# Performance work log

Hardware: AMD Instinct MI355X
Metric: run time of the kernel (lower is better)

Reference implementation:

```python
import jax, jax.numpy as jnp
import numpy as np

V_PATCH = (1, 2, 4, 8, 16, 32)
RESI = 0.5   # abs(quant_resi)
BETA = 0.25
K_PHI = 4    # share_quant_resi


def _phi_idx(si, SN, K=K_PHI):
    # PhiPartiallyShared.__getitem__ with at = si/(SN-1)
    ticks = np.linspace(1/3/K, 1 - 1/3/K, K) if K == 4 else np.linspace(1/2/K, 1 - 1/2/K, K)
    return int(np.argmin(np.abs(ticks - si / (SN - 1))))


def _area_down(x, pn):
    # F.interpolate mode='area' with pn | H  == exact block mean
    B, C, H, W = x.shape
    return x.reshape(B, C, pn, H // pn, pn, W // pn).mean(axis=(3, 5))


def _bilinear(x, size):
    # matches torch bilinear, align_corners=False, antialias=False (half-pixel centers)
    B, C, _, _ = x.shape
    return jax.image.resize(x, (B, C, size, size), method='bilinear', antialias=False)


def _down(x, pn, si):
    if pn == x.shape[2]:
        return x
    return _area_down(x, pn) if si <= 3 else _bilinear(x, pn)


def _phi_ada(h, w, b, fw, fb, sn):
    # Phi_ada: conv weight modulated by fc(SN); fc is zero-init but kept in the graph
    C = h.shape[1]
    cond = (fw[:, 0] * jnp.float32(sn) + fb).reshape(C, C, 1, 1)
    wmod = w * (1.0 + cond)
    y = jax.lax.conv_general_dilated(h, wmod, (1, 1), 'SAME',
                                     dimension_numbers=('NCHW', 'OIHW', 'NCHW'))
    y = y + b[None, :, None, None]
    return h * (1.0 - RESI) + y * RESI


def _forward(f, embed_w, conv_w, conv_b, fc_w, fc_b):
    B, C, H, W = f.shape
    SN = len(V_PATCH)
    f_ng = jax.lax.stop_gradient(f)
    f_rest = f_ng
    f_hat = jnp.zeros_like(f_ng)
    e_ng = jax.lax.stop_gradient(embed_w)            # embedding.weight.data
    e_sq = jnp.sum(e_ng * e_ng, axis=1)              # [V]
    vq_losses = []
    commit = jnp.float32(0.0)
    for si, pn in enumerate(V_PATCH):
        rest = f_rest if si == SN - 1 else _down(f_rest, pn, si)
        rest_NC = rest.transpose(0, 2, 3, 1).reshape(-1, C)          # [N,C]
        # squared L2 distances to codebook, argmin (non-differentiable)
        d = (jnp.sum(rest_NC * rest_NC, axis=1, keepdims=True)
             + e_sq - 2.0 * (rest_NC @ e_ng.T))                       # [N,V]
        idx = jnp.argmin(d, axis=1)                                   # [N]
        h = embed_w[idx].reshape(B, pn, pn, C).transpose(0, 3, 1, 2)  # [B,C,pn,pn]
        if si != SN - 1:
            h = _bilinear(h, H)
        k = _phi_idx(si, SN)
        h = _phi_ada(h, conv_w[k], conv_b[k], fc_w[k], fc_b[k], SN)
        f_hat = f_hat + h
        f_rest = f_rest - jax.lax.stop_gradient(h)    # grad through f_rest is killed by argmin anyway
        vq_losses.append(jnp.mean((f_hat - f_ng) ** 2))
        fh_ng = jax.lax.stop_gradient(f_hat)
        commit = commit + jnp.mean((_down(fh_ng, pn, si) - _down(f, pn, si)) ** 2) * BETA
    commit = commit / SN
    # straight-through estimator
    f_hat_out = jax.lax.stop_gradient(f_hat) - f_ng + f
    return f_hat_out, jnp.stack(vq_losses), commit


def setup_inputs() -> dict:
    key = jax.random.key(0)
    k1, k2, k3 = jax.random.split(key, 3)
    B, C, H, W = 32, 64, 32, 32
    V = 4096
    f_BChw = jax.random.normal(k1, (B, C, H, W), dtype=jnp.float32)
    embed_w = jax.random.normal(k2, (V, C), dtype=jnp.float32) * 0.5  # trunc_normal std=0.5
    conv_w = jax.random.normal(k3, (K_PHI, C, C, 3, 3), dtype=jnp.float32) * 0.02
    conv_b = jnp.zeros((K_PHI, C), dtype=jnp.float32)
    fc_w = jnp.zeros((K_PHI, C * C, 1), dtype=jnp.float32)  # Phi_ada.fc zero-init
    fc_b = jnp.zeros((K_PHI, C * C), dtype=jnp.float32)
    return {'f_BChw': f_BChw, 'embed_w': embed_w, 'conv_w': conv_w,
            'conv_b': conv_b, 'fc_w': fc_w, 'fc_b': fc_b}


def reference(f_BChw, embed_w, conv_w, conv_b, fc_w, fc_b):
    return _forward(f_BChw, embed_w, conv_w, conv_b, fc_w, fc_b)
```

## Files before the change

kernel.cpp:

```cpp
#include <hip/hip_runtime.h>
#include <cfloat>

#define N_ELEM 2097152
#define TAU 2.0e-2f

typedef short s16x8 __attribute__((ext_vector_type(8)));
typedef float f32x4 __attribute__((ext_vector_type(4)));

__device__ __forceinline__ unsigned short f2bf(float v) {
    unsigned u = __float_as_uint(v);
    u += 0x7FFFu + ((u >> 16) & 1u);
    return (unsigned short)(u >> 16);
}
__device__ __forceinline__ float bf2f(unsigned short h) {
    return __uint_as_float(((unsigned)h) << 16);
}

__device__ __forceinline__ float blockReduceSum(float v) {
    __shared__ float red[4];
    #pragma unroll
    for (int off = 32; off; off >>= 1) v += __shfl_down(v, off, 64);
    int wid = threadIdx.x >> 6, lane = threadIdx.x & 63;
    if (lane == 0) red[wid] = v;
    __syncthreads();
    float r = 0.f;
    if (threadIdx.x == 0) {
        int nw = ((int)blockDim.x + 63) >> 6;
        for (int w = 0; w < nw; ++w) r += red[w];
    }
    __syncthreads();
    return r;
}

__global__ void k_embprep(const float* __restrict__ e, float* __restrict__ hesq,
                          unsigned short* __restrict__ ehi, unsigned short* __restrict__ elo) {
    int v = blockIdx.x * 256 + threadIdx.x;
    if (v >= 4096) return;
    const float4* r = (const float4*)(e + (size_t)v * 64);
    float s = 0.f;
    #pragma unroll
    for (int i = 0; i < 16; ++i) {
        float4 a = r[i];
        s += a.x * a.x + a.y * a.y + a.z * a.z + a.w * a.w;
    }
    hesq[v] = 0.5f * s;
    for (int i = 0; i < 64; ++i) {
        float x = e[(size_t)v * 64 + i];
        unsigned short h = f2bf(x);
        ehi[(size_t)v * 64 + i] = h;
        elo[(size_t)v * 64 + i] = f2bf(x - bf2f(h));
    }
}

__global__ void k_wmod(const float* __restrict__ w, const float* __restrict__ fcw,
                       const float* __restrict__ fcb,
                       unsigned short* __restrict__ wh, unsigned short* __restrict__ wl) {
    int i = blockIdx.x * 256 + threadIdx.x;
    if (i >= 4 * 64 * 64 * 9) return;
    int k = i / (64 * 64 * 9);
    int r = i % (64 * 64 * 9);
    int oi = r / 9;
    int t = r % 9;
    int co = oi >> 6, ci = oi & 63;
    float cond = fcw[k * 4096 + oi] * 6.0f + fcb[k * 4096 + oi];
    float v = w[i] * (1.0f + cond);
    size_t o = ((size_t)(k * 9 + t) * 64 + co) * 64 + ci;
    unsigned short h = f2bf(v);
    wh[o] = h;
    wl[o] = f2bf(v - bf2f(h));
}

template<bool DIFF>
__global__ void k_pool_wide(const float* __restrict__ A, const float* __restrict__ Bt,
                            float* __restrict__ out, int pn, int s) {
    int o = blockIdx.x;
    int px = o % pn;
    int t1 = o / pn;
    int py = t1 % pn;
    int t2 = t1 / pn;
    int c = t2 % 64, b = t2 / 64;
    size_t base = (((size_t)(b * 64 + c)) * 32 + (size_t)py * s) * 32 + (size_t)px * s;
    float acc = 0.f;
    int tot = s * s;
    for (int i = threadIdx.x; i < tot; i += blockDim.x) {
        int dy = i / s, dx = i % s;
        float v = A[base + dy * 32 + dx];
        if (DIFF) v -= Bt[base + dy * 32 + dx];
        acc += v;
    }
    acc = blockReduceSum(acc);
    if (threadIdx.x == 0) out[o] = acc / (float)tot;
}

template<bool DIFF>
__global__ void k_pool_small(const float* __restrict__ A, const float* __restrict__ Bt,
                             float* __restrict__ out, int pn, int s) {
    int o = blockIdx.x * 256 + threadIdx.x;
    int total = 2048 * pn * pn;
    if (o >= total) return;
    int px = o % pn;
    int t1 = o / pn;
    int py = t1 % pn;
    int t2 = t1 / pn;
    int c = t2 % 64, b = t2 / 64;
    size_t base = (((size_t)(b * 64 + c)) * 32 + (size_t)py * s) * 32 + (size_t)px * s;
    float acc = 0.f;
    for (int dy = 0; dy < s; ++dy)
        for (int dx = 0; dx < s; ++dx) {
            float v = A[base + dy * 32 + dx];
            if (DIFF) v -= Bt[base + dy * 32 + dx];
            acc += v;
        }
    out[o] = acc / (float)(s * s);
}

__global__ void k_trans_nc(const float* __restrict__ src, float* __restrict__ dst,
                           unsigned short* __restrict__ dhi, unsigned short* __restrict__ dlo,
                           int pn2) {
    __shared__ float t[64][65];
    int b = blockIdx.x;
    int p0 = blockIdx.y * 64;
    int lane = threadIdx.x & 63, r4 = threadIdx.x >> 6;
    #pragma unroll
    for (int i = 0; i < 16; ++i) {
        int c = i * 4 + r4;
        t[c][lane] = src[((size_t)b * 64 + c) * pn2 + p0 + lane];
    }
    __syncthreads();
    #pragma unroll
    for (int i = 0; i < 16; ++i) {
        int p = i * 4 + r4;
        size_t o = ((size_t)(b * pn2 + p0 + p)) * 64 + lane;
        float v = t[lane][p];
        unsigned short h = f2bf(v);
        dst[o] = v;
        dhi[o] = h;
        dlo[o] = f2bf(v - bf2f(h));
    }
}

__global__ void k_trans_small(const float* __restrict__ src, float* __restrict__ dst,
                              unsigned short* __restrict__ dhi, unsigned short* __restrict__ dlo,
                              int pn2) {
    int i = blockIdx.x * 256 + threadIdx.x;
    int total = 2048 * pn2;
    if (i >= total) return;
    int c = i & 63, n = i >> 6;
    int b = n / pn2, p = n % pn2;
    float v = src[((size_t)b * 64 + c) * pn2 + p];
    unsigned short h = f2bf(v);
    dst[i] = v;
    dhi[i] = h;
    dlo[i] = f2bf(v - bf2f(h));
}

__global__ __launch_bounds__(256) void k_vq_mfma(
        const unsigned short* __restrict__ resthi, const unsigned short* __restrict__ restlo,
        const unsigned short* __restrict__ embhi,  const unsigned short* __restrict__ emblo,
        const float* __restrict__ hesq,
        float* __restrict__ m1v_, int* __restrict__ m1i_,
        float* __restrict__ m2v_, int* __restrict__ m2i_,
        int N, int CPS) {
    __shared__ __align__(16) unsigned short lah[64 * 64];
    __shared__ __align__(16) unsigned short lal[64 * 64];
    __shared__ __align__(16) float lq[64];
    int tid = threadIdx.x;
    int lane = tid & 63, wv = tid >> 6;
    int split = blockIdx.y;
    int p0 = blockIdx.x * 64 + wv * 16;
    int pt = p0 + (lane & 15);
    int ptc = min(pt, N - 1);
    int ko8 = (lane >> 4) * 8;

    const unsigned short* rb = resthi + (size_t)ptc * 64;
    const unsigned short* rl = restlo + (size_t)ptc * 64;
    s16x8 bh0 = *(const s16x8*)(rb + ko8);
    s16x8 bh1 = *(const s16x8*)(rb + 32 + ko8);
    s16x8 bl0 = *(const s16x8*)(rl + ko8);
    s16x8 bl1 = *(const s16x8*)(rl + 32 + ko8);

    float m1v = FLT_MAX, m2v = FLT_MAX;
    int m1i = 0, m2i = 0;

    int cbeg = split * CPS;
    for (int oc = 0; oc < CPS; oc += 64) {
        int cb = cbeg + oc;
        __syncthreads();
        for (int t = tid; t < 512; t += 256) {
            int cc = t >> 3, part = t & 7;
            int bo = (cc * 128 + part * 16) ^ ((cc & 7) << 4);
            *(uint4*)((char*)lah + bo) = *(const uint4*)(embhi + (size_t)(cb + cc) * 64 + part * 8);
            *(uint4*)((char*)lal + bo) = *(const uint4*)(emblo + (size_t)(cb + cc) * 64 + part * 8);
        }
        if (tid < 64) lq[tid] = hesq[cb + tid];
        __syncthreads();
        #pragma unroll
        for (int sub = 0; sub < 4; ++sub) {
            int cl = sub * 16 + (lane & 15);
            int sw = (cl & 7) << 4;
            int rowb = cl * 128;
            s16x8 ah0 = *(const s16x8*)((const char*)lah + ((rowb + ko8 * 2) ^ sw));
            s16x8 ah1 = *(const s16x8*)((const char*)lah + ((rowb + 64 + ko8 * 2) ^ sw));
            s16x8 al0 = *(const s16x8*)((const char*)lal + ((rowb + ko8 * 2) ^ sw));
            s16x8 al1 = *(const s16x8*)((const char*)lal + ((rowb + 64 + ko8 * 2) ^ sw));
            f32x4 acc = {0.f, 0.f, 0.f, 0.f};
            acc = __builtin_amdgcn_mfma_f32_16x16x32_bf16(ah0, bh0, acc, 0, 0, 0);
            acc = __builtin_amdgcn_mfma_f32_16x16x32_bf16(ah1, bh1, acc, 0, 0, 0);
            acc = __builtin_amdgcn_mfma_f32_16x16x32_bf16(ah0, bl0, acc, 0, 0, 0);
            acc = __builtin_amdgcn_mfma_f32_16x16x32_bf16(ah1, bl1, acc, 0, 0, 0);
            acc = __builtin_amdgcn_mfma_f32_16x16x32_bf16(al0, bh0, acc, 0, 0, 0);
            acc = __builtin_amdgcn_mfma_f32_16x16x32_bf16(al1, bh1, acc, 0, 0, 0);
            int crow = cb + sub * 16 + (lane >> 4) * 4;
            f32x4 q = *(const f32x4*)(lq + sub * 16 + (lane >> 4) * 4);
            #pragma unroll
            for (int r = 0; r < 4; ++r) {
                float s = q[r] - acc[r];
                int c = crow + r;
                bool lt1 = s < m1v, lt2 = s < m2v;
                float nm2v = lt2 ? s : m2v; int nm2i = lt2 ? c : m2i;
                nm2v = lt1 ? m1v : nm2v;    nm2i = lt1 ? m1i : nm2i;
                m1v = lt1 ? s : m1v;        m1i = lt1 ? c : m1i;
                m2v = nm2v; m2i = nm2i;
            }
        }
    }
    #pragma unroll
    for (int off = 16; off <= 32; off <<= 1) {
        float o1v = __shfl_xor(m1v, off, 64); int o1i = __shfl_xor(m1i, off, 64);
        float o2v = __shfl_xor(m2v, off, 64); int o2i = __shfl_xor(m2i, off, 64);
        if (o1v < m1v) {
            float c2v = (m1v < o2v) ? m1v : o2v; int c2i = (m1v < o2v) ? m1i : o2i;
            m1v = o1v; m1i = o1i; m2v = c2v; m2i = c2i;
        } else if (o1v < m2v) {
            m2v = o1v; m2i = o1i;
        }
    }
    if ((lane >> 4) == 0 && pt < N) {
        size_t o = (size_t)split * N + pt;
        m1v_[o] = m1v; m1i_[o] = m1i; m2v_[o] = m2v; m2i_[o] = m2i;
    }
}

__global__ void k_vq_combine(const float* __restrict__ m1v_, const int* __restrict__ m1i_,
                             const float* __restrict__ m2v_, const int* __restrict__ m2i_,
                             int* __restrict__ idx, int* __restrict__ flag, int* __restrict__ count,
                             int N, int SPLITS) {
    int n = blockIdx.x * 256 + threadIdx.x;
    if (n >= N) return;
    float a1v = m1v_[n], a2v = m2v_[n];
    int a1i = m1i_[n], a2i = m2i_[n];
    for (int s = 1; s < SPLITS; ++s) {
        size_t o = (size_t)s * N + n;
        float b1v = m1v_[o], b2v = m2v_[o];
        int b1i = m1i_[o], b2i = m2i_[o];
        if (b1v < a1v) {
            float c2v = (a1v < b2v) ? a1v : b2v; int c2i = (a1v < b2v) ? a1i : b2i;
            a1v = b1v; a1i = b1i; a2v = c2v; a2i = c2i;
        } else if (b1v < a2v) {
            a2v = b1v; a2i = b1i;
        }
    }
    idx[n] = a1i;
    if (a2v - a1v < TAU) {
        int p = atomicAdd(count, 1);
        flag[p] = n;
    }
}

__global__ __launch_bounds__(256) void k_vq_exact(
        const float* __restrict__ restnc, const float* __restrict__ embed,
        const float* __restrict__ hesq, const int* __restrict__ flag,
        const int* __restrict__ count, unsigned long long* __restrict__ pmin) {
    __shared__ float rs[32 * 64];
    __shared__ unsigned long long red[4];
    int tid = threadIdx.x;
    int lane = tid & 63, wv = tid >> 6;
    int cnt = *count;
    int nb = (cnt + 31) >> 5;
    int ntask = nb * 16;
    for (int task = blockIdx.x; task < ntask; task += gridDim.x) {
        int batch = task >> 4, spl = task & 15;
        int lbase = batch << 5;
        int npts = min(32, cnt - lbase);
        __syncthreads();
        for (int i = tid; i < npts * 64; i += 256) {
            int li = i >> 6;
            rs[i] = restnc[(size_t)flag[lbase + li] * 64 + (i & 63)];
        }
        __syncthreads();
        int code = spl * 256 + tid;
        const float4* e4 = (const float4*)(embed + (size_t)code * 64);
        float4 e[16];
        #pragma unroll
        for (int i = 0; i < 16; ++i) e[i] = e4[i];
        float hq = hesq[code];
        for (int p = 0; p < npts; ++p) {
            const float4* r4 = (const float4*)(rs + p * 64);
            float d0 = 0.f, d1 = 0.f, d2 = 0.f, d3 = 0.f;
            #pragma unroll
            for (int i = 0; i < 16; i += 4) {
                float4 e0 = e[i], e1 = e[i + 1], e2 = e[i + 2], e3 = e[i + 3];
                d0 += e0.x * r4[i].x     + e0.y * r4[i].y     + e0.z * r4[i].z     + e0.w * r4[i].w;
                d1 += e1.x * r4[i + 1].x + e1.y * r4[i + 1].y + e1.z * r4[i + 1].z + e1.w * r4[i + 1].w;
                d2 += e2.x * r4[i + 2].x + e2.y * r4[i + 2].y + e2.z * r4[i + 2].z + e2.w * r4[i + 2].w;
                d3 += e3.x * r4[i + 3].x + e3.y * r4[i + 3].y + e3.z * r4[i + 3].z + e3.w * r4[i + 3].w;
            }
            float s = hq - ((d0 + d1) + (d2 + d3));
            unsigned u = __float_as_uint(s);
            u = (u & 0x80000000u) ? ~u : (u | 0x80000000u);
            unsigned long long pk = (((unsigned long long)u) << 32) | (unsigned)code;
            #pragma unroll
            for (int off = 32; off; off >>= 1) {
                unsigned long long o = __shfl_down(pk, off, 64);
                if (o < pk) pk = o;
            }
            if (lane == 0) red[wv] = pk;
            __syncthreads();
            if (tid == 0) {
                unsigned long long m = red[0];
                for (int w = 1; w < 4; ++w) if (red[w] < m) m = red[w];
                atomicMin(pmin + flag[lbase + p], m);
            }
            __syncthreads();
        }
    }
}

__global__ void k_gather(const int* __restrict__ idx, const unsigned long long* __restrict__ pmin,
                         const float* __restrict__ embed, float* __restrict__ hs, int N) {
    int i = blockIdx.x * 256 + threadIdx.x;
    if (i >= N * 64) return;
    int n = i >> 6, c = i & 63;
    unsigned long long pv = pmin[n];
    int id = (pv != 0xFFFFFFFFFFFFFFFFull) ? (int)(pv & 0xFFFFFFFFull) : idx[n];
    hs[i] = embed[(size_t)id * 64 + c];
}

__global__ void k_upsample(const float* __restrict__ hs, float* __restrict__ hupf,
                           unsigned short* __restrict__ huph, unsigned short* __restrict__ hupl,
                           int pn) {
    int i = blockIdx.x * 256 + threadIdx.x;
    if (i >= N_ELEM) return;
    int c = i & 63, x = (i >> 6) & 31, y = (i >> 11) & 31, b = i >> 16;
    float scale = (float)pn * (1.0f / 32.0f);
    float sy = (y + 0.5f) * scale - 0.5f;
    float sx = (x + 0.5f) * scale - 0.5f;
    float fy0 = floorf(sy), fx0 = floorf(sx);
    float wy = sy - fy0, wx = sx - fx0;
    int y0 = max(0, min(pn - 1, (int)fy0));
    int y1 = max(0, min(pn - 1, (int)fy0 + 1));
    int x0 = max(0, min(pn - 1, (int)fx0));
    int x1 = max(0, min(pn - 1, (int)fx0 + 1));
    const float* hb = hs + (size_t)b * pn * pn * 64 + c;
    float v00 = hb[(size_t)(y0 * pn + x0) * 64];
    float v01 = hb[(size_t)(y0 * pn + x1) * 64];
    float v10 = hb[(size_t)(y1 * pn + x0) * 64];
    float v11 = hb[(size_t)(y1 * pn + x1) * 64];
    float v = (1.f - wy) * ((1.f - wx) * v00 + wx * v01) + wy * ((1.f - wx) * v10 + wx * v11);
    hupf[i] = v;
    unsigned short h = f2bf(v);
    huph[i] = h;
    hupl[i] = f2bf(v - bf2f(h));
}

__global__ void k_hilo(const float* __restrict__ hs,
                       unsigned short* __restrict__ huph, unsigned short* __restrict__ hupl) {
    int i = blockIdx.x * 256 + threadIdx.x;
    if (i >= N_ELEM) return;
    float v = hs[i];
    unsigned short h = f2bf(v);
    huph[i] = h;
    hupl[i] = f2bf(v - bf2f(h));
}

__global__ __launch_bounds__(256) void k_conv_mfma(
        const unsigned short* __restrict__ huph, const unsigned short* __restrict__ hupl,
        const float* __restrict__ hupf,
        const unsigned short* __restrict__ wh, const unsigned short* __restrict__ wl,
        const float* __restrict__ bias, const float* __restrict__ f_in,
        float* __restrict__ f_hat, float* __restrict__ f_rest,
        float* __restrict__ vq_part) {
    __shared__ __align__(16) unsigned short Xh[6 * 34 * 64];
    __shared__ __align__(16) unsigned short Xl[6 * 34 * 64];
    int b = blockIdx.x, rg = blockIdx.y;
    int y0 = rg * 4;
    int tid = threadIdx.x;
    int lane = tid & 63, wv = tid >> 6;
    int co0 = wv * 16;
    int cr = lane & 15, oct = lane >> 4;

    for (int q = tid; q < 6 * 34 * 8; q += 256) {
        int pl = q >> 3, o8 = q & 7;
        int lr = pl / 34, lc = pl % 34;
        int gy = y0 + lr - 1, gx = lc - 1;
        int bo = (pl * 128 + o8 * 16) ^ ((lc & 7) << 4);
        uint4 vh = {0, 0, 0, 0}, vl = {0, 0, 0, 0};
        if (gy >= 0 && gy < 32 && gx >= 0 && gx < 32) {
            size_t g = (((size_t)(b * 32 + gy)) * 32 + gx) * 64 + o8 * 8;
            vh = *(const uint4*)(huph + g);
            vl = *(const uint4*)(hupl + g);
        }
        *(uint4*)((char*)Xh + bo) = vh;
        *(uint4*)((char*)Xl + bo) = vl;
    }
    __syncthreads();

    f32x4 acc[8];
    #pragma unroll
    for (int ps = 0; ps < 8; ++ps) acc[ps] = (f32x4){0.f, 0.f, 0.f, 0.f};

    for (int t = 0; t < 9; ++t) {
        int dy = t / 3, dx = t % 3;
        #pragma unroll
        for (int cc = 0; cc < 2; ++cc) {
            size_t wo = ((size_t)t * 64 + co0 + cr) * 64 + cc * 32 + oct * 8;
            s16x8 Ah = *(const s16x8*)(wh + wo);
            s16x8 Al = *(const s16x8*)(wl + wo);
            #pragma unroll
            for (int ps = 0; ps < 8; ++ps) {
                int px = ps * 16 + cr;
                int lr = (px >> 5) + dy;
                int lc = (px & 31) + dx;
                int bo = ((lr * 34 + lc) * 128 + cc * 64 + oct * 16) ^ ((lc & 7) << 4);
                s16x8 Bh = *(const s16x8*)((const char*)Xh + bo);
                s16x8 Bl = *(const s16x8*)((const char*)Xl + bo);
                acc[ps] = __builtin_amdgcn_mfma_f32_16x16x32_bf16(Ah, Bh, acc[ps], 0, 0, 0);
                acc[ps] = __builtin_amdgcn_mfma_f32_16x16x32_bf16(Ah, Bl, acc[ps], 0, 0, 0);
                acc[ps] = __builtin_amdgcn_mfma_f32_16x16x32_bf16(Al, Bh, acc[ps], 0, 0, 0);
                acc[ps] = __builtin_amdgcn_mfma_f32_16x16x32_bf16(Al, Bl, acc[ps], 0, 0, 0);
            }
        }
    }

    const float* hupb = hupf + (size_t)b * 65536;
    float local = 0.f;
    #pragma unroll
    for (int ps = 0; ps < 8; ++ps) {
        int px = ps * 16 + cr;
        int y = y0 + (px >> 5), x = px & 31;
        #pragma unroll
        for (int r = 0; r < 4; ++r) {
            int co = co0 + oct * 4 + r;
            float hv = hupb[(size_t)(y * 32 + x) * 64 + co];
            float hconv = acc[ps][r] + bias[co];
            float hout = 0.5f * hv + 0.5f * hconv;
            size_t o = (((size_t)(b * 64 + co)) * 32 + y) * 32 + x;
            float fh = f_hat[o] + hout;
            f_hat[o] = fh;
            f_rest[o] -= hout;
            float d = fh - f_in[o];
            local += d * d;
        }
    }
    local = blockReduceSum(local);
    if (tid == 0) vq_part[b * 8 + rg] = local;
}

__global__ void k_sqsum(const float* __restrict__ v, float* __restrict__ part, int M) {
    float local = 0.f;
    for (int i = blockIdx.x * 256 + threadIdx.x; i < M; i += gridDim.x * 256) {
        float a = v[i];
        local += a * a;
    }
    local = blockReduceSum(local);
    if (threadIdx.x == 0) part[blockIdx.x] = local;
}

__global__ void k_final(const float* __restrict__ vqp, const float* __restrict__ cmp,
                        float* __restrict__ out) {
    const int pn2s[6] = {1, 4, 16, 64, 256, 1024};
    float commit = 0.f;
    for (int si = 0; si < 6; ++si) {
        float l = (threadIdx.x < 256) ? vqp[si * 256 + threadIdx.x] : 0.f;
        l = blockReduceSum(l);
        if (threadIdx.x == 0) out[N_ELEM + si] = l / (float)N_ELEM;

        float csum = 0.f;
        for (int i = threadIdx.x; i < 512; i += 256) csum += cmp[si * 512 + i];
        csum = blockReduceSum(csum);
        if (threadIdx.x == 0) commit += csum / (float)(2048 * pn2s[si]) * 0.25f;
    }
    if (threadIdx.x == 0) out[N_ELEM + 6] = commit / 6.0f;
}

extern "C" void kernel_launch(void* const* d_in, const int* in_sizes, int n_in,
                              void* d_out, int out_size, void* d_ws, size_t ws_size,
                              hipStream_t stream) {
    const float* f     = (const float*)d_in[0];
    const float* embed = (const float*)d_in[1];
    const float* convw = (const float*)d_in[2];
    const float* convb = (const float*)d_in[3];
    const float* fcw   = (const float*)d_in[4];
    const float* fcb   = (const float*)d_in[5];
    float* out = (float*)d_out;
    float* ws  = (float*)d_ws;

    float* f_rest  = ws;
    float* poolhup = ws + 2097152;
    float* restnc  = ws + 4194304;
    float* hs      = restnc;
    unsigned short* resthi = (unsigned short*)(ws + 6291456);
    unsigned short* restlo = (unsigned short*)(ws + 7340032);
    unsigned short* huph   = resthi;
    unsigned short* hupl   = restlo;
    unsigned short* embhi  = (unsigned short*)(ws + 8388608);
    unsigned short* emblo  = (unsigned short*)(ws + 8519680);
    unsigned short* wmodh  = (unsigned short*)(ws + 8650752);
    unsigned short* wmodl  = (unsigned short*)(ws + 8724480);
    float* hesq   = ws + 8798208;
    float* m1v    = ws + 8802304;
    float* m2v    = ws + 8867840;
    int*   m1i    = (int*)(ws + 8933376);
    int*   m2i    = (int*)(ws + 8998912);
    int*   idx    = (int*)(ws + 9064448);
    int*   flag   = (int*)(ws + 9097216);
    int*   count  = (int*)(ws + 9129984);
    unsigned long long* pmin = (unsigned long long*)(ws + 9130048);
    float* vqp    = ws + 9195584;
    float* cmp    = ws + 9197120;

    hipMemsetAsync(d_out, 0, (size_t)out_size * sizeof(float), stream);
    hipMemcpyAsync(f_rest, f, (size_t)N_ELEM * sizeof(float), hipMemcpyDeviceToDevice, stream);
    k_wmod<<<(147456 + 255) / 256, 256, 0, stream>>>(convw, fcw, fcb, wmodh, wmodl);
    k_embprep<<<16, 256, 0, stream>>>(embed, hesq, embhi, emblo);

    const int pns[6]    = {1, 2, 4, 8, 16, 32};
    const int splits[6] = {64, 32, 16, 8, 4, 2};
    const int kidx[6]   = {0, 0, 1, 2, 3, 3};

    for (int si = 0; si < 6; ++si) {
        int pn = pns[si], s = 32 / pn, pn2 = pn * pn;
        int N = 32 * pn2, SPL = splits[si], CPS = 4096 / SPL;
        float* pooled = poolhup;
        float* hupf = poolhup;

        if (si <= 2) {
            k_pool_wide<false><<<2048 * pn2, (s >= 16 ? 256 : 64), 0, stream>>>(f_rest, nullptr, pooled, pn, s);
            k_trans_small<<<(N * 64 + 255) / 256, 256, 0, stream>>>(pooled, restnc, resthi, restlo, pn2);
        } else if (si <= 4) {
            k_pool_small<false><<<(2048 * pn2 + 255) / 256, 256, 0, stream>>>(f_rest, nullptr, pooled, pn, s);
            k_trans_nc<<<dim3(32, pn2 / 64), 256, 0, stream>>>(pooled, restnc, resthi, restlo, pn2);
        } else {
            k_trans_nc<<<dim3(32, 16), 256, 0, stream>>>(f_rest, restnc, resthi, restlo, 1024);
        }

        hipMemsetAsync(count, 0, sizeof(int), stream);
        hipMemsetAsync(pmin, 0xFF, (size_t)N * 8, stream);
        k_vq_mfma<<<dim3((N + 63) / 64, SPL), 256, 0, stream>>>(resthi, restlo, embhi, emblo, hesq,
                                                                m1v, m1i, m2v, m2i, N, CPS);
        k_vq_combine<<<(N + 255) / 256, 256, 0, stream>>>(m1v, m1i, m2v, m2i, idx, flag, count, N, SPL);
        k_vq_exact<<<1024, 256, 0, stream>>>(restnc, embed, hesq, flag, count, pmin);

        k_gather<<<(N * 64 + 255) / 256, 256, 0, stream>>>(idx, pmin, embed, hs, N);
        if (si < 5) {
            k_upsample<<<(N_ELEM + 255) / 256, 256, 0, stream>>>(hs, hupf, huph, hupl, pn);
        } else {
            k_hilo<<<(N_ELEM + 255) / 256, 256, 0, stream>>>(hs, huph, hupl);
            hupf = hs;
        }

        k_conv_mfma<<<dim3(32, 8), 256, 0, stream>>>(huph, hupl, hupf,
                                                     wmodh + kidx[si] * 36864, wmodl + kidx[si] * 36864,
                                                     convb + kidx[si] * 64, f, out, f_rest,
                                                     vqp + si * 256);

        if (si <= 2) k_pool_wide<true><<<2048 * pn2, (s >= 16 ? 256 : 64), 0, stream>>>(out, f, pooled, pn, s);
        else         k_pool_small<true><<<(2048 * pn2 + 255) / 256, 256, 0, stream>>>(out, f, pooled, pn, s);
        k_sqsum<<<512, 256, 0, stream>>>(pooled, cmp + si * 512, 2048 * pn2);
    }

    k_final<<<1, 256, 0, stream>>>(vqp, cmp, out);
}
```

Before: 715.9 us.

## Fuse residual computation, gather/upsample, commit reductions; widen VQ tile to two point groups

```diff
diff --git a/kernel.cpp b/kernel.cpp
--- a/kernel.cpp
+++ b/kernel.cpp
@@ -33,7 +33,7 @@
 }
 
 __global__ void k_embprep(const float* __restrict__ e, float* __restrict__ hesq,
-                          unsigned short* __restrict__ ehi, unsigned short* __restrict__ elo) {
+                          unsigned short* __restrict__ ehiN, unsigned short* __restrict__ eloN) {
     int v = blockIdx.x * 256 + threadIdx.x;
     if (v >= 4096) return;
     const float4* r = (const float4*)(e + (size_t)v * 64);
@@ -47,16 +47,22 @@
     for (int i = 0; i < 64; ++i) {
         float x = e[(size_t)v * 64 + i];
         unsigned short h = f2bf(x);
-        ehi[(size_t)v * 64 + i] = h;
-        elo[(size_t)v * 64 + i] = f2bf(x - bf2f(h));
+        ehiN[(size_t)v * 64 + i] = h ^ 0x8000u;
+        eloN[(size_t)v * 64 + i] = f2bf(x - bf2f(h)) ^ 0x8000u;
     }
 }
 
 __global__ void k_wmod(const float* __restrict__ w, const float* __restrict__ fcw,
                        const float* __restrict__ fcb,
-                       unsigned short* __restrict__ wh, unsigned short* __restrict__ wl) {
+                       unsigned short* __restrict__ wh, unsigned short* __restrict__ wl,
+                       int* __restrict__ count, float* __restrict__ cmpA) {
+    if (blockIdx.x == 576) {
+        int t = threadIdx.x;
+        for (int j = t; j < 384; j += 256) cmpA[j] = 0.f;
+        if (t < 6) count[t] = 0;
+        return;
+    }
     int i = blockIdx.x * 256 + threadIdx.x;
-    if (i >= 4 * 64 * 64 * 9) return;
     int k = i / (64 * 64 * 9);
     int r = i % (64 * 64 * 9);
     int oi = r / 9;
@@ -70,9 +76,9 @@
     wl[o] = f2bf(v - bf2f(h));
 }
 
-template<bool DIFF>
-__global__ void k_pool_wide(const float* __restrict__ A, const float* __restrict__ Bt,
-                            float* __restrict__ out, int pn, int s) {
+__global__ void k_down_wide(const float* __restrict__ f, const float* __restrict__ fhat,
+                            float* __restrict__ restnc, unsigned short* __restrict__ dhi,
+                            unsigned short* __restrict__ dlo, int pn, int s) {
     int o = blockIdx.x;
     int px = o % pn;
     int t1 = o / pn;
@@ -84,16 +90,21 @@
     int tot = s * s;
     for (int i = threadIdx.x; i < tot; i += blockDim.x) {
         int dy = i / s, dx = i % s;
-        float v = A[base + dy * 32 + dx];
-        if (DIFF) v -= Bt[base + dy * 32 + dx];
-        acc += v;
+        acc += f[base + dy * 32 + dx] - fhat[base + dy * 32 + dx];
     }
     acc = blockReduceSum(acc);
-    if (threadIdx.x == 0) out[o] = acc / (float)tot;
-}
-
-template<bool DIFF>
-__global__ void k_pool_small(const float* __restrict__ A, const float* __restrict__ Bt,
+    if (threadIdx.x == 0) {
+        float v = acc / (float)tot;
+        int n = (b * pn + py) * pn + px;
+        size_t oo = (size_t)n * 64 + c;
+        unsigned short h = f2bf(v);
+        restnc[oo] = v;
+        dhi[oo] = h;
+        dlo[oo] = f2bf(v - bf2f(h));
+    }
+}
+
+__global__ void k_pool_small(const float* __restrict__ f, const float* __restrict__ fhat,
                              float* __restrict__ out, int pn, int s) {
     int o = blockIdx.x * 256 + threadIdx.x;
     int total = 2048 * pn * pn;
@@ -106,15 +117,14 @@
     size_t base = (((size_t)(b * 64 + c)) * 32 + (size_t)py * s) * 32 + (size_t)px * s;
     float acc = 0.f;
     for (int dy = 0; dy < s; ++dy)
-        for (int dx = 0; dx < s; ++dx) {
-            float v = A[base + dy * 32 + dx];
-            if (DIFF) v -= Bt[base + dy * 32 + dx];
-            acc += v;
-        }
+        for (int dx = 0; dx < s; ++dx)
+            acc += f[base + dy * 32 + dx] - fhat[base + dy * 32 + dx];
     out[o] = acc / (float)(s * s);
 }
 
-__global__ void k_trans_nc(const float* __restrict__ src, float* __restrict__ dst,
+template<bool DIFF>
+__global__ void k_trans_nc(const float* __restrict__ A, const float* __restrict__ Bt,
+                           float* __restrict__ dst,
                            unsigned short* __restrict__ dhi, unsigned short* __restrict__ dlo,
                            int pn2) {
     __shared__ float t[64][65];
@@ -124,7 +134,10 @@
     #pragma unroll
     for (int i = 0; i < 16; ++i) {
         int c = i * 4 + r4;
-        t[c][lane] = src[((size_t)b * 64 + c) * pn2 + p0 + lane];
+        size_t g = ((size_t)b * 64 + c) * pn2 + p0 + lane;
+        float v = A[g];
+        if (DIFF) v -= Bt[g];
+        t[c][lane] = v;
     }
     __syncthreads();
     #pragma unroll
@@ -139,27 +152,11 @@
     }
 }
 
-__global__ void k_trans_small(const float* __restrict__ src, float* __restrict__ dst,
-                              unsigned short* __restrict__ dhi, unsigned short* __restrict__ dlo,
-                              int pn2) {
-    int i = blockIdx.x * 256 + threadIdx.x;
-    int total = 2048 * pn2;
-    if (i >= total) return;
-    int c = i & 63, n = i >> 6;
-    int b = n / pn2, p = n % pn2;
-    float v = src[((size_t)b * 64 + c) * pn2 + p];
-    unsigned short h = f2bf(v);
-    dst[i] = v;
-    dhi[i] = h;
-    dlo[i] = f2bf(v - bf2f(h));
-}
-
 __global__ __launch_bounds__(256) void k_vq_mfma(
         const unsigned short* __restrict__ resthi, const unsigned short* __restrict__ restlo,
-        const unsigned short* __restrict__ embhi,  const unsigned short* __restrict__ emblo,
+        const unsigned short* __restrict__ embhiN, const unsigned short* __restrict__ embloN,
         const float* __restrict__ hesq,
-        float* __restrict__ m1v_, int* __restrict__ m1i_,
-        float* __restrict__ m2v_, int* __restrict__ m2i_,
+        float* __restrict__ m1v_, int* __restrict__ m1i_, float* __restrict__ m2v_,
         int N, int CPS) {
     __shared__ __align__(16) unsigned short lah[64 * 64];
     __shared__ __align__(16) unsigned short lal[64 * 64];
@@ -167,20 +164,27 @@
     int tid = threadIdx.x;
     int lane = tid & 63, wv = tid >> 6;
     int split = blockIdx.y;
-    int p0 = blockIdx.x * 64 + wv * 16;
-    int pt = p0 + (lane & 15);
-    int ptc = min(pt, N - 1);
-    int ko8 = (lane >> 4) * 8;
-
-    const unsigned short* rb = resthi + (size_t)ptc * 64;
-    const unsigned short* rl = restlo + (size_t)ptc * 64;
-    s16x8 bh0 = *(const s16x8*)(rb + ko8);
-    s16x8 bh1 = *(const s16x8*)(rb + 32 + ko8);
-    s16x8 bl0 = *(const s16x8*)(rl + ko8);
-    s16x8 bl1 = *(const s16x8*)(rl + 32 + ko8);
-
-    float m1v = FLT_MAX, m2v = FLT_MAX;
-    int m1i = 0, m2i = 0;
+    int p0 = blockIdx.x * 128 + wv * 32;
+    int cr = lane & 15, oct = lane >> 4;
+    int ko8 = oct * 8;
+    int ptA = p0 + cr, ptB = p0 + 16 + cr;
+    int pA = min(ptA, N - 1), pB = min(ptB, N - 1);
+
+    const unsigned short* ra = resthi + (size_t)pA * 64;
+    const unsigned short* la = restlo + (size_t)pA * 64;
+    const unsigned short* rb = resthi + (size_t)pB * 64;
+    const unsigned short* lb = restlo + (size_t)pB * 64;
+    s16x8 bhA0 = *(const s16x8*)(ra + ko8);
+    s16x8 bhA1 = *(const s16x8*)(ra + 32 + ko8);
+    s16x8 blA0 = *(const s16x8*)(la + ko8);
+    s16x8 blA1 = *(const s16x8*)(la + 32 + ko8);
+    s16x8 bhB0 = *(const s16x8*)(rb + ko8);
+    s16x8 bhB1 = *(const s16x8*)(rb + 32 + ko8);
+    s16x8 blB0 = *(const s16x8*)(lb + ko8);
+    s16x8 blB1 = *(const s16x8*)(lb + 32 + ko8);
+
+    float m1vA = FLT_MAX, m2vA = FLT_MAX; int m1iA = 0;
+    float m1vB = FLT_MAX, m2vB = FLT_MAX; int m1iB = 0;
 
     int cbeg = split * CPS;
     for (int oc = 0; oc < CPS; oc += 64) {
@@ -189,78 +193,94 @@
         for (int t = tid; t < 512; t += 256) {
             int cc = t >> 3, part = t & 7;
             int bo = (cc * 128 + part * 16) ^ ((cc & 7) << 4);
-            *(uint4*)((char*)lah + bo) = *(const uint4*)(embhi + (size_t)(cb + cc) * 64 + part * 8);
-            *(uint4*)((char*)lal + bo) = *(const uint4*)(emblo + (size_t)(cb + cc) * 64 + part * 8);
+            *(uint4*)((char*)lah + bo) = *(const uint4*)(embhiN + (size_t)(cb + cc) * 64 + part * 8);
+            *(uint4*)((char*)lal + bo) = *(const uint4*)(embloN + (size_t)(cb + cc) * 64 + part * 8);
         }
         if (tid < 64) lq[tid] = hesq[cb + tid];
         __syncthreads();
         #pragma unroll
         for (int sub = 0; sub < 4; ++sub) {
-            int cl = sub * 16 + (lane & 15);
+            int cl = sub * 16 + cr;
             int sw = (cl & 7) << 4;
             int rowb = cl * 128;
             s16x8 ah0 = *(const s16x8*)((const char*)lah + ((rowb + ko8 * 2) ^ sw));
             s16x8 ah1 = *(const s16x8*)((const char*)lah + ((rowb + 64 + ko8 * 2) ^ sw));
             s16x8 al0 = *(const s16x8*)((const char*)lal + ((rowb + ko8 * 2) ^ sw));
             s16x8 al1 = *(const s16x8*)((const char*)lal + ((rowb + 64 + ko8 * 2) ^ sw));
-            f32x4 acc = {0.f, 0.f, 0.f, 0.f};
-            acc = __builtin_amdgcn_mfma_f32_16x16x32_bf16(ah0, bh0, acc, 0, 0, 0);
-            acc = __builtin_amdgcn_mfma_f32_16x16x32_bf16(ah1, bh1, acc, 0, 0, 0);
-            acc = __builtin_amdgcn_mfma_f32_16x16x32_bf16(ah0, bl0, acc, 0, 0, 0);
-            acc = __builtin_amdgcn_mfma_f32_16x16x32_bf16(ah1, bl1, acc, 0, 0, 0);
-            acc = __builtin_amdgcn_mfma_f32_16x16x32_bf16(al0, bh0, acc, 0, 0, 0);
-            acc = __builtin_amdgcn_mfma_f32_16x16x32_bf16(al1, bh1, acc, 0, 0, 0);
-            int crow = cb + sub * 16 + (lane >> 4) * 4;
-            f32x4 q = *(const f32x4*)(lq + sub * 16 + (lane >> 4) * 4);
+            f32x4 q = *(const f32x4*)(lq + sub * 16 + oct * 4);
+            int crow = cb + sub * 16 + oct * 4;
+            f32x4 acc = q;
+            acc = __builtin_amdgcn_mfma_f32_16x16x32_bf16(ah0, bhA0, acc, 0, 0, 0);
+            acc = __builtin_amdgcn_mfma_f32_16x16x32_bf16(ah1, bhA1, acc, 0, 0, 0);
+            acc = __builtin_amdgcn_mfma_f32_16x16x32_bf16(ah0, blA0, acc, 0, 0, 0);
+            acc = __builtin_amdgcn_mfma_f32_16x16x32_bf16(ah1, blA1, acc, 0, 0, 0);
+            acc = __builtin_amdgcn_mfma_f32_16x16x32_bf16(al0, bhA0, acc, 0, 0, 0);
+            acc = __builtin_amdgcn_mfma_f32_16x16x32_bf16(al1, bhA1, acc, 0, 0, 0);
             #pragma unroll
             for (int r = 0; r < 4; ++r) {
-                float s = q[r] - acc[r];
-                int c = crow + r;
-                bool lt1 = s < m1v, lt2 = s < m2v;
-                float nm2v = lt2 ? s : m2v; int nm2i = lt2 ? c : m2i;
-                nm2v = lt1 ? m1v : nm2v;    nm2i = lt1 ? m1i : nm2i;
-                m1v = lt1 ? s : m1v;        m1i = lt1 ? c : m1i;
-                m2v = nm2v; m2i = nm2i;
+                float s = acc[r]; int c = crow + r;
+                bool lt1 = s < m1vA, lt2 = s < m2vA;
+                float nm2 = lt2 ? s : m2vA;
+                m2vA = lt1 ? m1vA : nm2;
+                m1iA = lt1 ? c : m1iA;
+                m1vA = lt1 ? s : m1vA;
+            }
+            f32x4 accB = q;
+            accB = __builtin_amdgcn_mfma_f32_16x16x32_bf16(ah0, bhB0, accB, 0, 0, 0);
+            accB = __builtin_amdgcn_mfma_f32_16x16x32_bf16(ah1, bhB1, accB, 0, 0, 0);
+            accB = __builtin_amdgcn_mfma_f32_16x16x32_bf16(ah0, blB0, accB, 0, 0, 0);
+            accB = __builtin_amdgcn_mfma_f32_16x16x32_bf16(ah1, blB1, accB, 0, 0, 0);
+            accB = __builtin_amdgcn_mfma_f32_16x16x32_bf16(al0, bhB0, accB, 0, 0, 0);
+            accB = __builtin_amdgcn_mfma_f32_16x16x32_bf16(al1, bhB1, accB, 0, 0, 0);
+            #pragma unroll
+            for (int r = 0; r < 4; ++r) {
+                float s = accB[r]; int c = crow + r;
+                bool lt1 = s < m1vB, lt2 = s < m2vB;
+                float nm2 = lt2 ? s : m2vB;
+                m2vB = lt1 ? m1vB : nm2;
+                m1iB = lt1 ? c : m1iB;
+                m1vB = lt1 ? s : m1vB;
             }
         }
     }
     #pragma unroll
     for (int off = 16; off <= 32; off <<= 1) {
-        float o1v = __shfl_xor(m1v, off, 64); int o1i = __shfl_xor(m1i, off, 64);
-        float o2v = __shfl_xor(m2v, off, 64); int o2i = __shfl_xor(m2i, off, 64);
-        if (o1v < m1v) {
-            float c2v = (m1v < o2v) ? m1v : o2v; int c2i = (m1v < o2v) ? m1i : o2i;
-            m1v = o1v; m1i = o1i; m2v = c2v; m2i = c2i;
-        } else if (o1v < m2v) {
-            m2v = o1v; m2i = o1i;
-        }
-    }
-    if ((lane >> 4) == 0 && pt < N) {
-        size_t o = (size_t)split * N + pt;
-        m1v_[o] = m1v; m1i_[o] = m1i; m2v_[o] = m2v; m2i_[o] = m2i;
+        float o1 = __shfl_xor(m1vA, off, 64); int oi = __shfl_xor(m1iA, off, 64);
+        float o2 = __shfl_xor(m2vA, off, 64);
+        if (o1 < m1vA) { m2vA = fminf(m1vA, o2); m1vA = o1; m1iA = oi; }
+        else if (o1 < m2vA) m2vA = o1;
+        o1 = __shfl_xor(m1vB, off, 64); oi = __shfl_xor(m1iB, off, 64);
+        o2 = __shfl_xor(m2vB, off, 64);
+        if (o1 < m1vB) { m2vB = fminf(m1vB, o2); m1vB = o1; m1iB = oi; }
+        else if (o1 < m2vB) m2vB = o1;
+    }
+    if (oct == 0) {
+        if (ptA < N) { size_t o = (size_t)split * N + ptA; m1v_[o] = m1vA; m1i_[o] = m1iA; m2v_[o] = m2vA; }
+        if (ptB < N) { size_t o = (size_t)split * N + ptB; m1v_[o] = m1vB; m1i_[o] = m1iB; m2v_[o] = m2vB; }
     }
 }
 
 __global__ void k_vq_combine(const float* __restrict__ m1v_, const int* __restrict__ m1i_,
-                             const float* __restrict__ m2v_, const int* __restrict__ m2i_,
+                             const float* __restrict__ m2v_,
                              int* __restrict__ idx, int* __restrict__ flag, int* __restrict__ count,
-                             int N, int SPLITS) {
+                             unsigned long long* __restrict__ pmin, int N, int SPLITS) {
     int n = blockIdx.x * 256 + threadIdx.x;
     if (n >= N) return;
     float a1v = m1v_[n], a2v = m2v_[n];
-    int a1i = m1i_[n], a2i = m2i_[n];
+    int a1i = m1i_[n];
     for (int s = 1; s < SPLITS; ++s) {
         size_t o = (size_t)s * N + n;
         float b1v = m1v_[o], b2v = m2v_[o];
-        int b1i = m1i_[o], b2i = m2i_[o];
+        int b1i = m1i_[o];
         if (b1v < a1v) {
-            float c2v = (a1v < b2v) ? a1v : b2v; int c2i = (a1v < b2v) ? a1i : b2i;
-            a1v = b1v; a1i = b1i; a2v = c2v; a2i = c2i;
+            a2v = fminf(a1v, b2v);
+            a1v = b1v; a1i = b1i;
         } else if (b1v < a2v) {
-            a2v = b1v; a2i = b1i;
+            a2v = b1v;
         }
     }
     idx[n] = a1i;
+    pmin[n] = 0xFFFFFFFFFFFFFFFFull;
     if (a2v - a1v < TAU) {
         int p = atomicAdd(count, 1);
         flag[p] = n;
@@ -272,9 +292,8 @@
         const float* __restrict__ hesq, const int* __restrict__ flag,
         const int* __restrict__ count, unsigned long long* __restrict__ pmin) {
     __shared__ float rs[32 * 64];
-    __shared__ unsigned long long red[4];
     int tid = threadIdx.x;
-    int lane = tid & 63, wv = tid >> 6;
+    int lane = tid & 63;
     int cnt = *count;
     int nb = (cnt + 31) >> 5;
     int ntask = nb * 16;
@@ -314,60 +333,49 @@
                 unsigned long long o = __shfl_down(pk, off, 64);
                 if (o < pk) pk = o;
             }
-            if (lane == 0) red[wv] = pk;
-            __syncthreads();
-            if (tid == 0) {
-                unsigned long long m = red[0];
-                for (int w = 1; w < 4; ++w) if (red[w] < m) m = red[w];
-                atomicMin(pmin + flag[lbase + p], m);
-            }
-            __syncthreads();
-        }
-    }
-}
-
-__global__ void k_gather(const int* __restrict__ idx, const unsigned long long* __restrict__ pmin,
-                         const float* __restrict__ embed, float* __restrict__ hs, int N) {
-    int i = blockIdx.x * 256 + threadIdx.x;
-    if (i >= N * 64) return;
-    int n = i >> 6, c = i & 63;
-    unsigned long long pv = pmin[n];
-    int id = (pv != 0xFFFFFFFFFFFFFFFFull) ? (int)(pv & 0xFFFFFFFFull) : idx[n];
-    hs[i] = embed[(size_t)id * 64 + c];
-}
-
-__global__ void k_upsample(const float* __restrict__ hs, float* __restrict__ hupf,
-                           unsigned short* __restrict__ huph, unsigned short* __restrict__ hupl,
-                           int pn) {
+            if (lane == 0) atomicMin(pmin + flag[lbase + p], pk);
+        }
+    }
+}
+
+__global__ void k_up(const int* __restrict__ idx, const unsigned long long* __restrict__ pmin,
+                     const float* __restrict__ embed, float* __restrict__ hupf,
+                     unsigned short* __restrict__ huph, unsigned short* __restrict__ hupl,
+                     int pn) {
     int i = blockIdx.x * 256 + threadIdx.x;
     if (i >= N_ELEM) return;
     int c = i & 63, x = (i >> 6) & 31, y = (i >> 11) & 31, b = i >> 16;
-    float scale = (float)pn * (1.0f / 32.0f);
-    float sy = (y + 0.5f) * scale - 0.5f;
-    float sx = (x + 0.5f) * scale - 0.5f;
-    float fy0 = floorf(sy), fx0 = floorf(sx);
-    float wy = sy - fy0, wx = sx - fx0;
-    int y0 = max(0, min(pn - 1, (int)fy0));
-    int y1 = max(0, min(pn - 1, (int)fy0 + 1));
-    int x0 = max(0, min(pn - 1, (int)fx0));
-    int x1 = max(0, min(pn - 1, (int)fx0 + 1));
-    const float* hb = hs + (size_t)b * pn * pn * 64 + c;
-    float v00 = hb[(size_t)(y0 * pn + x0) * 64];
-    float v01 = hb[(size_t)(y0 * pn + x1) * 64];
-    float v10 = hb[(size_t)(y1 * pn + x0) * 64];
-    float v11 = hb[(size_t)(y1 * pn + x1) * 64];
-    float v = (1.f - wy) * ((1.f - wx) * v00 + wx * v01) + wy * ((1.f - wx) * v10 + wx * v11);
+    float v;
+    if (pn == 32) {
+        int n = (b * 32 + y) * 32 + x;
+        unsigned long long pv = pmin[n];
+        int id = (pv != 0xFFFFFFFFFFFFFFFFull) ? (int)(pv & 0xFFFFFFFFull) : idx[n];
+        v = embed[(size_t)id * 64 + c];
+    } else {
+        float scale = (float)pn * (1.0f / 32.0f);
+        float sy = (y + 0.5f) * scale - 0.5f;
+        float sx = (x + 0.5f) * scale - 0.5f;
+        float fy0 = floorf(sy), fx0 = floorf(sx);
+        float wy = sy - fy0, wx = sx - fx0;
+        int y0 = max(0, min(pn - 1, (int)fy0));
+        int y1 = max(0, min(pn - 1, (int)fy0 + 1));
+        int x0 = max(0, min(pn - 1, (int)fx0));
+        int x1 = max(0, min(pn - 1, (int)fx0 + 1));
+        int nb_ = b * pn * pn;
+        int n00 = nb_ + y0 * pn + x0, n01 = nb_ + y0 * pn + x1;
+        int n10 = nb_ + y1 * pn + x0, n11 = nb_ + y1 * pn + x1;
+        unsigned long long p00 = pmin[n00], p01 = pmin[n01], p10 = pmin[n10], p11 = pmin[n11];
+        int i00 = (p00 != 0xFFFFFFFFFFFFFFFFull) ? (int)(p00 & 0xFFFFFFFFull) : idx[n00];
+        int i01 = (p01 != 0xFFFFFFFFFFFFFFFFull) ? (int)(p01 & 0xFFFFFFFFull) : idx[n01];
+        int i10 = (p10 != 0xFFFFFFFFFFFFFFFFull) ? (int)(p10 & 0xFFFFFFFFull) : idx[n10];
+        int i11 = (p11 != 0xFFFFFFFFFFFFFFFFull) ? (int)(p11 & 0xFFFFFFFFull) : idx[n11];
+        float v00 = embed[(size_t)i00 * 64 + c];
+        float v01 = embed[(size_t)i01 * 64 + c];
+        float v10 = embed[(size_t)i10 * 64 + c];
+        float v11 = embed[(size_t)i11 * 64 + c];
+        v = (1.f - wy) * ((1.f - wx) * v00 + wx * v01) + wy * ((1.f - wx) * v10 + wx * v11);
+    }
     hupf[i] = v;
-    unsigned short h = f2bf(v);
-    huph[i] = h;
-    hupl[i] = f2bf(v - bf2f(h));
-}
-
-__global__ void k_hilo(const float* __restrict__ hs,
-                       unsigned short* __restrict__ huph, unsigned short* __restrict__ hupl) {
-    int i = blockIdx.x * 256 + threadIdx.x;
-    if (i >= N_ELEM) return;
-    float v = hs[i];
     unsigned short h = f2bf(v);
     huph[i] = h;
     hupl[i] = f2bf(v - bf2f(h));
@@ -378,8 +386,7 @@
         const float* __restrict__ hupf,
         const unsigned short* __restrict__ wh, const unsigned short* __restrict__ wl,
         const float* __restrict__ bias, const float* __restrict__ f_in,
-        float* __restrict__ f_hat, float* __restrict__ f_rest,
-        float* __restrict__ vq_part) {
+        float* __restrict__ f_hat, float* __restrict__ vq_part) {
     __shared__ __align__(16) unsigned short Xh[6 * 34 * 64];
     __shared__ __align__(16) unsigned short Xl[6 * 34 * 64];
     int b = blockIdx.x, rg = blockIdx.y;
@@ -447,7 +454,6 @@
             size_t o = (((size_t)(b * 64 + co)) * 32 + y) * 32 + x;
             float fh = f_hat[o] + hout;
             f_hat[o] = fh;
-            f_rest[o] -= hout;
             float d = fh - f_in[o];
             local += d * d;
         }
@@ -456,31 +462,73 @@
     if (tid == 0) vq_part[b * 8 + rg] = local;
 }
 
-__global__ void k_sqsum(const float* __restrict__ v, float* __restrict__ part, int M) {
-    float local = 0.f;
-    for (int i = blockIdx.x * 256 + threadIdx.x; i < M; i += gridDim.x * 256) {
-        float a = v[i];
-        local += a * a;
-    }
-    local = blockReduceSum(local);
-    if (threadIdx.x == 0) part[blockIdx.x] = local;
-}
-
-__global__ void k_final(const float* __restrict__ vqp, const float* __restrict__ cmp,
+__global__ void k_commit_wide(const float* __restrict__ fhat, const float* __restrict__ f,
+                              float* __restrict__ cmp, int pn, int s) {
+    int o = blockIdx.x;
+    int px = o % pn;
+    int t1 = o / pn;
+    int py = t1 % pn;
+    int t2 = t1 / pn;
+    int c = t2 % 64, b = t2 / 64;
+    size_t base = (((size_t)(b * 64 + c)) * 32 + (size_t)py * s) * 32 + (size_t)px * s;
+    float acc = 0.f;
+    int tot = s * s;
+    for (int i = threadIdx.x; i < tot; i += blockDim.x) {
+        int dy = i / s, dx = i % s;
+        acc += fhat[base + dy * 32 + dx] - f[base + dy * 32 + dx];
+    }
+    acc = blockReduceSum(acc);
+    if (threadIdx.x == 0) {
+        float m = acc / (float)tot;
+        atomicAdd(cmp + (blockIdx.x & 63), m * m);
+    }
+}
+
+__global__ void k_commit_small(const float* __restrict__ fhat, const float* __restrict__ f,
+                               float* __restrict__ cmp, int pn, int s) {
+    int o = blockIdx.x * 256 + threadIdx.x;
+    int total = 2048 * pn * pn;
+    float m2 = 0.f;
+    if (o < total) {
+        int px = o % pn;
+        int t1 = o / pn;
+        int py = t1 % pn;
+        int t2 = t1 / pn;
+        int c = t2 % 64, b = t2 / 64;
+        size_t base = (((size_t)(b * 64 + c)) * 32 + (size_t)py * s) * 32 + (size_t)px * s;
+        float acc = 0.f;
+        for (int dy = 0; dy < s; ++dy)
+            for (int dx = 0; dx < s; ++dx)
+                acc += fhat[base + dy * 32 + dx] - f[base + dy * 32 + dx];
+        float m = acc / (float)(s * s);
+        m2 = m * m;
+    }
+    m2 = blockReduceSum(m2);
+    if (threadIdx.x == 0) atomicAdd(cmp + (blockIdx.x & 63), m2);
+}
+
+__global__ void k_final(const float* __restrict__ vqp, const float* __restrict__ cmpA,
                         float* __restrict__ out) {
-    const int pn2s[6] = {1, 4, 16, 64, 256, 1024};
-    float commit = 0.f;
+    const int pn2s[5] = {1, 4, 16, 64, 256};
+    __shared__ float commit_s;
+    if (threadIdx.x == 0) commit_s = 0.f;
+    __syncthreads();
     for (int si = 0; si < 6; ++si) {
-        float l = (threadIdx.x < 256) ? vqp[si * 256 + threadIdx.x] : 0.f;
+        float l = vqp[si * 256 + threadIdx.x];
         l = blockReduceSum(l);
-        if (threadIdx.x == 0) out[N_ELEM + si] = l / (float)N_ELEM;
-
-        float csum = 0.f;
-        for (int i = threadIdx.x; i < 512; i += 256) csum += cmp[si * 512 + i];
-        csum = blockReduceSum(csum);
-        if (threadIdx.x == 0) commit += csum / (float)(2048 * pn2s[si]) * 0.25f;
-    }
-    if (threadIdx.x == 0) out[N_ELEM + 6] = commit / 6.0f;
+        if (threadIdx.x == 0) {
+            float vl = l / (float)N_ELEM;
+            out[N_ELEM + si] = vl;
+            if (si == 5) commit_s += vl * 0.25f;
+        }
+        if (si < 5) {
+            float csum = (threadIdx.x < 64) ? cmpA[si * 64 + threadIdx.x] : 0.f;
+            csum = blockReduceSum(csum);
+            if (threadIdx.x == 0) commit_s += csum / (float)(2048 * pn2s[si]) * 0.25f;
+        }
+    }
+    __syncthreads();
+    if (threadIdx.x == 0) out[N_ELEM + 6] = commit_s / 6.0f;
 }
 
 extern "C" void kernel_launch(void* const* d_in, const int* in_sizes, int n_in,
@@ -495,79 +543,63 @@
     float* out = (float*)d_out;
     float* ws  = (float*)d_ws;
 
-    float* f_rest  = ws;
-    float* poolhup = ws + 2097152;
-    float* restnc  = ws + 4194304;
-    float* hs      = restnc;
-    unsigned short* resthi = (unsigned short*)(ws + 6291456);
-    unsigned short* restlo = (unsigned short*)(ws + 7340032);
+    float* hupf   = ws;
+    float* restnc = ws + 2097152;
+    unsigned short* resthi = (unsigned short*)(ws + 4194304);
+    unsigned short* restlo = (unsigned short*)(ws + 5242880);
     unsigned short* huph   = resthi;
     unsigned short* hupl   = restlo;
-    unsigned short* embhi  = (unsigned short*)(ws + 8388608);
-    unsigned short* emblo  = (unsigned short*)(ws + 8519680);
-    unsigned short* wmodh  = (unsigned short*)(ws + 8650752);
-    unsigned short* wmodl  = (unsigned short*)(ws + 8724480);
-    float* hesq   = ws + 8798208;
-    float* m1v    = ws + 8802304;
-    float* m2v    = ws + 8867840;
-    int*   m1i    = (int*)(ws + 8933376);
-    int*   m2i    = (int*)(ws + 8998912);
-    int*   idx    = (int*)(ws + 9064448);
-    int*   flag   = (int*)(ws + 9097216);
-    int*   count  = (int*)(ws + 9129984);
-    unsigned long long* pmin = (unsigned long long*)(ws + 9130048);
-    float* vqp    = ws + 9195584;
-    float* cmp    = ws + 9197120;
+    unsigned short* embhiN = (unsigned short*)(ws + 6291456);
+    unsigned short* embloN = (unsigned short*)(ws + 6422528);
+    unsigned short* wmodh  = (unsigned short*)(ws + 6553600);
+    unsigned short* wmodl  = (unsigned short*)(ws + 6627328);
+    float* hesq   = ws + 6701056;
+    float* m1v    = ws + 6705152;
+    float* m2v    = ws + 6836224;
+    int*   m1i    = (int*)(ws + 6967296);
+    int*   idx    = (int*)(ws + 7098368);
+    int*   flag   = (int*)(ws + 7131136);
+    int*   count  = (int*)(ws + 7163904);
+    unsigned long long* pmin = (unsigned long long*)(ws + 7163968);
+    float* vqp    = ws + 7229504;
+    float* cmpA   = ws + 7231040;
 
     hipMemsetAsync(d_out, 0, (size_t)out_size * sizeof(float), stream);
-    hipMemcpyAsync(f_rest, f, (size_t)N_ELEM * sizeof(float), hipMemcpyDeviceToDevice, stream);
-    k_wmod<<<(147456 + 255) / 256, 256, 0, stream>>>(convw, fcw, fcb, wmodh, wmodl);
-    k_embprep<<<16, 256, 0, stream>>>(embed, hesq, embhi, emblo);
+    k_wmod<<<577, 256, 0, stream>>>(convw, fcw, fcb, wmodh, wmodl, count, cmpA);
+    k_embprep<<<16, 256, 0, stream>>>(embed, hesq, embhiN, embloN);
 
     const int pns[6]    = {1, 2, 4, 8, 16, 32};
-    const int splits[6] = {64, 32, 16, 8, 4, 2};
+    const int splits[6] = {64, 64, 32, 16, 8, 4};
     const int kidx[6]   = {0, 0, 1, 2, 3, 3};
 
     for (int si = 0; si < 6; ++si) {
         int pn = pns[si], s = 32 / pn, pn2 = pn * pn;
         int N = 32 * pn2, SPL = splits[si], CPS = 4096 / SPL;
-        float* pooled = poolhup;
-        float* hupf = poolhup;
+        float* pooled = hupf;
 
         if (si <= 2) {
-            k_pool_wide<false><<<2048 * pn2, (s >= 16 ? 256 : 64), 0, stream>>>(f_rest, nullptr, pooled, pn, s);
-            k_trans_small<<<(N * 64 + 255) / 256, 256, 0, stream>>>(pooled, restnc, resthi, restlo, pn2);
+            k_down_wide<<<2048 * pn2, (s == 32 ? 256 : 64), 0, stream>>>(f, out, restnc, resthi, restlo, pn, s);
         } else if (si <= 4) {
-            k_pool_small<false><<<(2048 * pn2 + 255) / 256, 256, 0, stream>>>(f_rest, nullptr, pooled, pn, s);
-            k_trans_nc<<<dim3(32, pn2 / 64), 256, 0, stream>>>(pooled, restnc, resthi, restlo, pn2);
+            k_pool_small<<<(2048 * pn2 + 255) / 256, 256, 0, stream>>>(f, out, pooled, pn, s);
+            k_trans_nc<false><<<dim3(32, pn2 / 64), 256, 0, stream>>>(pooled, nullptr, restnc, resthi, restlo, pn2);
         } else {
-            k_trans_nc<<<dim3(32, 16), 256, 0, stream>>>(f_rest, restnc, resthi, restlo, 1024);
-        }
-
-        hipMemsetAsync(count, 0, sizeof(int), stream);
-        hipMemsetAsync(pmin, 0xFF, (size_t)N * 8, stream);
-        k_vq_mfma<<<dim3((N + 63) / 64, SPL), 256, 0, stream>>>(resthi, restlo, embhi, emblo, hesq,
-                                                                m1v, m1i, m2v, m2i, N, CPS);
-        k_vq_combine<<<(N + 255) / 256, 256, 0, stream>>>(m1v, m1i, m2v, m2i, idx, flag, count, N, SPL);
-        k_vq_exact<<<1024, 256, 0, stream>>>(restnc, embed, hesq, flag, count, pmin);
-
-        k_gather<<<(N * 64 + 255) / 256, 256, 0, stream>>>(idx, pmin, embed, hs, N);
-        if (si < 5) {
-            k_upsample<<<(N_ELEM + 255) / 256, 256, 0, stream>>>(hs, hupf, huph, hupl, pn);
-        } else {
-            k_hilo<<<(N_ELEM + 255) / 256, 256, 0, stream>>>(hs, huph, hupl);
-            hupf = hs;
-        }
+            k_trans_nc<true><<<dim3(32, 16), 256, 0, stream>>>(f, out, restnc, resthi, restlo, 1024);
+        }
+
+        k_vq_mfma<<<dim3((N + 127) / 128, SPL), 256, 0, stream>>>(resthi, restlo, embhiN, embloN, hesq,
+                                                                  m1v, m1i, m2v, N, CPS);
+        k_vq_combine<<<(N + 255) / 256, 256, 0, stream>>>(m1v, m1i, m2v, idx, flag, count + si, pmin, N, SPL);
+        k_vq_exact<<<512, 256, 0, stream>>>(restnc, embed, hesq, flag, count + si, pmin);
+
+        k_up<<<(N_ELEM + 255) / 256, 256, 0, stream>>>(idx, pmin, embed, hupf, huph, hupl, pn);
 
         k_conv_mfma<<<dim3(32, 8), 256, 0, stream>>>(huph, hupl, hupf,
                                                      wmodh + kidx[si] * 36864, wmodl + kidx[si] * 36864,
-                                                     convb + kidx[si] * 64, f, out, f_rest,
-                                                     vqp + si * 256);
-
-        if (si <= 2) k_pool_wide<true><<<2048 * pn2, (s >= 16 ? 256 : 64), 0, stream>>>(out, f, pooled, pn, s);
-        else         k_pool_small<true><<<(2048 * pn2 + 255) / 256, 256, 0, stream>>>(out, f, pooled, pn, s);
-        k_sqsum<<<512, 256, 0, stream>>>(pooled, cmp + si * 512, 2048 * pn2);
-    }
-
-    k_final<<<1, 256, 0, stream>>>(vqp, cmp, out);
-}
+                                                     convb + kidx[si] * 64, f, out, vqp + si * 256);
+
+        if (si <= 2)      k_commit_wide<<<2048 * pn2, (s == 32 ? 256 : 64), 0, stream>>>(out, f, cmpA + si * 64, pn, s);
+        else if (si <= 4) k_commit_small<<<(2048 * pn2 + 255) / 256, 256, 0, stream>>>(out, f, cmpA + si * 64, pn, s);
+    }
+
+    k_final<<<1, 256, 0, stream>>>(vqp, cmpA, out);
+}
```

After: 911.1 us. 1.27x slower.
